# Performance work log

Measured on AMD Instinct MI355X. Metric: run time of the kernel, lower is better.

Reference implementation:

```python
import jax, jax.numpy as jnp
import numpy as np

D_MODEL = 2048
H = 8
DK = D_MODEL // H          # 256
EXPAND = 2
D_INNER = EXPAND * D_MODEL  # 4096
D_STATE = 16
D_CONV = 4
DT_RANK = D_MODEL // 16     # 128
B_SZ = 8
L = 1024


def setup_inputs() -> dict:
    key = jax.random.key(0)
    ks = jax.random.split(key, 20)
    s = 0.02
    inp = {
        "imageFeature": jax.random.normal(ks[0], (B_SZ, L, D_MODEL), jnp.float32),
        "kf": jax.random.normal(ks[1], (B_SZ, L, D_MODEL), jnp.float32),
        # MHA params (4 linears with bias)
        "Wq": jax.random.normal(ks[2], (D_MODEL, D_MODEL), jnp.float32) * s,
        "bq": jnp.zeros((D_MODEL,), jnp.float32),
        "Wk": jax.random.normal(ks[3], (D_MODEL, D_MODEL), jnp.float32) * s,
        "bk": jnp.zeros((D_MODEL,), jnp.float32),
        "Wv": jax.random.normal(ks[4], (D_MODEL, D_MODEL), jnp.float32) * s,
        "bv": jnp.zeros((D_MODEL,), jnp.float32),
        "Wo": jax.random.normal(ks[5], (D_MODEL, D_MODEL), jnp.float32) * s,
        "bo": jnp.zeros((D_MODEL,), jnp.float32),
        # Mamba params
        "W_in": jax.random.normal(ks[6], (D_MODEL, 2 * D_INNER), jnp.float32) * s,
        "conv_w": jax.random.normal(ks[7], (D_INNER, D_CONV), jnp.float32) * s,
        "conv_b": jnp.zeros((D_INNER,), jnp.float32),
        "W_extra": jax.random.normal(ks[8], (D_MODEL, D_INNER), jnp.float32) * s,
        "W_xproj": jax.random.normal(ks[9], (D_INNER, DT_RANK + 2 * D_STATE), jnp.float32) * s,
        "W_dt": jax.random.normal(ks[10], (DT_RANK, D_INNER), jnp.float32) * s,
        "b_dt": jnp.full((D_INNER,), -4.6, jnp.float32),  # softplus(-4.6) ~ 0.01 init dt
        "A_log": jnp.log(jnp.broadcast_to(jnp.arange(1, D_STATE + 1, dtype=jnp.float32), (D_INNER, D_STATE))),
        "D_skip": jnp.ones((D_INNER,), jnp.float32),
        "W_out": jax.random.normal(ks[11], (D_INNER, D_MODEL), jnp.float32) * s,
    }
    return inp


def _mha(x, Wq, bq, Wk, bk, Wv, bv, Wo, bo):
    B, T, _ = x.shape
    q = (x @ Wq + bq).reshape(B, T, H, DK)
    k = (x @ Wk + bk).reshape(B, T, H, DK)
    v = (x @ Wv + bv).reshape(B, T, H, DK)
    scores = jnp.einsum("bqhd,bkhd->bhqk", q, k) / jnp.sqrt(jnp.float32(DK))
    attn = jax.nn.softmax(scores, axis=-1)
    out = jnp.einsum("bhqk,bkhd->bqhd", attn, v).reshape(B, T, D_MODEL)
    return out @ Wo + bo


def _mamba_cross(x_in, kf, W_in, conv_w, conv_b, W_extra, W_xproj, W_dt, b_dt, A_log, D_skip, W_out):
    B, T, _ = x_in.shape
    xz = x_in @ W_in                       # (B,T,2*D_INNER)
    x, z = jnp.split(xz, 2, axis=-1)
    # causal depthwise conv1d (kernel D_CONV)
    x_pad = jnp.pad(x, ((0, 0), (D_CONV - 1, 0), (0, 0)))
    x_conv = sum(conv_w[:, k] * x_pad[:, k:k + T, :] for k in range(D_CONV)) + conv_b
    x = jax.nn.silu(x_conv)               # (B,T,D_INNER)
    # dt/B/C conditioned on extra_emb (cross path)
    e = kf @ W_extra                       # (B,T,D_INNER)
    dbc = e @ W_xproj                      # (B,T,DT_RANK+2*D_STATE)
    dt = jax.nn.softplus(dbc[..., :DT_RANK] @ W_dt + b_dt)        # (B,T,D_INNER)
    Bt = dbc[..., DT_RANK:DT_RANK + D_STATE]                      # (B,T,N)
    Ct = dbc[..., DT_RANK + D_STATE:]                             # (B,T,N)
    A = -jnp.exp(A_log)                    # (D_INNER, D_STATE)

    def step(h, inputs):
        x_t, dt_t, B_t, C_t = inputs       # (B,D),(B,D),(B,N),(B,N)
        dA = jnp.exp(dt_t[..., None] * A)              # (B,D,N)
        h = dA * h + dt_t[..., None] * B_t[:, None, :] * x_t[..., None]
        y_t = jnp.einsum("bdn,bn->bd", h, C_t)
        return h, y_t

    h0 = jnp.zeros((B, D_INNER, D_STATE), x.dtype)
    xs = (x.transpose(1, 0, 2), dt.transpose(1, 0, 2),
          Bt.transpose(1, 0, 2), Ct.transpose(1, 0, 2))
    _, ys = jax.lax.scan(step, h0, xs)     # ys: (T,B,D_INNER)
    y = ys.transpose(1, 0, 2) + D_skip * x
    y = y * jax.nn.silu(z)
    return y @ W_out


def reference(imageFeature, kf, Wq, bq, Wk, bk, Wv, bv, Wo, bo,
              W_in, conv_w, conv_b, W_extra, W_xproj, W_dt, b_dt,
              A_log, D_skip, W_out):
    att_feats = _mha(imageFeature, Wq, bq, Wk, bk, Wv, bv, Wo, bo)
    src = _mamba_cross(imageFeature, kf, W_in, conv_w, conv_b, W_extra,
                       W_xproj, W_dt, b_dt, A_log, D_skip, W_out)
    return jnp.stack([att_feats, src])     # (2,B,T,D_MODEL)
```

## Files before the change

kernel.cpp:

```cpp
#include <hip/hip_runtime.h>
#include <math.h>

#define NH 8
#define DKH 256
#define SEQ 1024
#define BSZ 8
#define DMODEL 2048
#define DINNER 4096
#define DSTATE 16
#define DTRANK 128

#define MiB 1048576ULL

#define O_XZ    (0*MiB)
#define O_IMGH  (256*MiB)
#define O_IMGL  (288*MiB)
#define O_WINTH (320*MiB)
#define O_WINTL (352*MiB)
#define O_WCOMB (384*MiB)
#define O_DBC   (384*MiB + 1310720ULL)
#define O_DT    (256*MiB)
#define O_YH    (256*MiB)
#define O_YL    (320*MiB)
#define O_WOUTH (0*MiB)
#define O_WOUTL (16*MiB)
#define A_IMGH  (0*MiB)
#define A_IMGL  (32*MiB)
#define A_WQH   (64*MiB)
#define A_WQL   (72*MiB)
#define A_WKH   (80*MiB)
#define A_WKL   (88*MiB)
#define A_WVH   (96*MiB)
#define A_WVL   (104*MiB)
#define A_WOH   (112*MiB)
#define A_WOL   (120*MiB)
#define A_QH    (128*MiB)
#define A_QL    (160*MiB)
#define A_KH    (192*MiB)
#define A_KL    (224*MiB)
#define A_VTH   (256*MiB)
#define A_VTL   (288*MiB)
#define A_S     (320*MiB)
#define A_ATTH  (0*MiB)
#define A_ATTL  (32*MiB)

#define FLAG_BIAS 1
#define FLAG_SOFTPLUS 2
#define FLAG_KT 4
#define FLAG_BF16 8

typedef __attribute__((ext_vector_type(8))) short bf16x8;
typedef __attribute__((ext_vector_type(4))) float f32x4;
typedef const void __attribute__((address_space(1))) gv_t;
typedef void __attribute__((address_space(3))) lv_t;

__device__ __forceinline__ unsigned short f2bf(float x) {
    unsigned u = __float_as_uint(x);
    unsigned r = u + 0x7FFFu + ((u >> 16) & 1u);
    return (unsigned short)(r >> 16);
}
__device__ __forceinline__ float bf2f(unsigned short h) {
    return __uint_as_float((unsigned)h << 16);
}

__global__ __launch_bounds__(256) void cvt_hilo(
    const float* __restrict__ in, unsigned short* __restrict__ hi,
    unsigned short* __restrict__ lo, int n4)
{
    int i = blockIdx.x * 256 + threadIdx.x;
    if (i >= n4) return;
    float4 x = ((const float4*)in)[i];
    ushort4 h, l;
    h.x = f2bf(x.x); l.x = f2bf(x.x - bf2f(h.x));
    h.y = f2bf(x.y); l.y = f2bf(x.y - bf2f(h.y));
    h.z = f2bf(x.z); l.z = f2bf(x.z - bf2f(h.z));
    h.w = f2bf(x.w); l.w = f2bf(x.w - bf2f(h.w));
    ((ushort4*)hi)[i] = h;
    ((ushort4*)lo)[i] = l;
}

__global__ __launch_bounds__(256) void tcvt(
    const float* __restrict__ W, unsigned short* __restrict__ Thi,
    unsigned short* __restrict__ Tlo, int K, int N)
{
    __shared__ float t[32][33];
    int tx = threadIdx.x & 31, ty = threadIdx.x >> 5;
    int k0 = blockIdx.y * 32, n0 = blockIdx.x * 32;
    #pragma unroll
    for (int i = 0; i < 32; i += 8)
        t[ty + i][tx] = W[(size_t)(k0 + ty + i) * N + n0 + tx];
    __syncthreads();
    #pragma unroll
    for (int i = 0; i < 32; i += 8) {
        float v = t[tx][ty + i];
        size_t o = (size_t)(n0 + ty + i) * K + k0 + tx;
        unsigned short h = f2bf(v);
        Thi[o] = h;
        Tlo[o] = f2bf(v - bf2f(h));
    }
}

__global__ __launch_bounds__(256) void ycvt(
    const float* __restrict__ xz, unsigned short* __restrict__ hi,
    unsigned short* __restrict__ lo)
{
    int i = blockIdx.x * 256 + threadIdx.x;
    int r = i >> 10, c4 = (i & 1023) << 2;
    float4 x = *(const float4*)&xz[(size_t)r * 8192 + c4];
    ushort4 h, l;
    h.x = f2bf(x.x); l.x = f2bf(x.x - bf2f(h.x));
    h.y = f2bf(x.y); l.y = f2bf(x.y - bf2f(h.y));
    h.z = f2bf(x.z); l.z = f2bf(x.z - bf2f(h.z));
    h.w = f2bf(x.w); l.w = f2bf(x.w - bf2f(h.w));
    size_t o = ((size_t)r * 4096 + c4) >> 2;
    ((ushort4*)hi)[o] = h;
    ((ushort4*)lo)[o] = l;
}

__device__ __forceinline__ void gload16(const unsigned short* g, unsigned short* l) {
    __builtin_amdgcn_global_load_lds((gv_t*)g, (lv_t*)l, 16, 0, 0);
}

__global__ __launch_bounds__(256) void gemm_mfma3(
    const unsigned short* __restrict__ Ahi, const unsigned short* __restrict__ Alo,
    const unsigned short* __restrict__ Bhi, const unsigned short* __restrict__ Blo,
    const float* __restrict__ bias, float* __restrict__ C,
    unsigned short* __restrict__ Chi, unsigned short* __restrict__ Clo,
    int M, int N, int K, int flags)
{
    __shared__ unsigned short sAh[128*32], sAl[128*32], sBh[128*32], sBl[128*32];
    int tid = threadIdx.x;
    int lane = tid & 63, wv = tid >> 6;
    int wm = wv >> 1, wn = wv & 1;
    int bm = blockIdx.y * 128, bn = blockIdx.x * 128;

    int rbase = wv * 32;
    int srow = lane >> 2;
    int scol = (lane & 3) * 8;
    const size_t aoff0 = (size_t)(bm + rbase + srow) * K + scol;
    const size_t aoff1 = aoff0 + (size_t)16 * K;
    const size_t boff0 = (size_t)(bn + rbase + srow) * K + scol;
    const size_t boff1 = boff0 + (size_t)16 * K;
    unsigned short* lA0 = &sAh[rbase * 32];
    unsigned short* lA1 = &sAh[(rbase + 16) * 32];
    unsigned short* lAl0 = &sAl[rbase * 32];
    unsigned short* lAl1 = &sAl[(rbase + 16) * 32];
    unsigned short* lB0 = &sBh[rbase * 32];
    unsigned short* lB1 = &sBh[(rbase + 16) * 32];
    unsigned short* lBl0 = &sBl[rbase * 32];
    unsigned short* lBl1 = &sBl[(rbase + 16) * 32];

    f32x4 acc[4][4];
    #pragma unroll
    for (int i = 0; i < 4; i++)
        #pragma unroll
        for (int j = 0; j < 4; j++)
            acc[i][j] = (f32x4){0.f, 0.f, 0.f, 0.f};

    int fr = lane & 15, q8 = (lane >> 4) * 8;

    for (int k0 = 0; k0 < K; k0 += 32) {
        gload16(Ahi + aoff0 + k0, lA0);
        gload16(Ahi + aoff1 + k0, lA1);
        gload16(Alo + aoff0 + k0, lAl0);
        gload16(Alo + aoff1 + k0, lAl1);
        gload16(Bhi + boff0 + k0, lB0);
        gload16(Bhi + boff1 + k0, lB1);
        gload16(Blo + boff0 + k0, lBl0);
        gload16(Blo + boff1 + k0, lBl1);
        __syncthreads();

        bf16x8 ah[4], al[4], bh[4], bl[4];
        #pragma unroll
        for (int t = 0; t < 4; t++) {
            ah[t] = *(const bf16x8*)&sAh[(wm * 64 + t * 16 + fr) * 32 + q8];
            al[t] = *(const bf16x8*)&sAl[(wm * 64 + t * 16 + fr) * 32 + q8];
            bh[t] = *(const bf16x8*)&sBh[(wn * 64 + t * 16 + fr) * 32 + q8];
            bl[t] = *(const bf16x8*)&sBl[(wn * 64 + t * 16 + fr) * 32 + q8];
        }
        #pragma unroll
        for (int i = 0; i < 4; i++)
            #pragma unroll
            for (int j = 0; j < 4; j++) {
                acc[i][j] = __builtin_amdgcn_mfma_f32_16x16x32_bf16(ah[i], bh[j], acc[i][j], 0, 0, 0);
                acc[i][j] = __builtin_amdgcn_mfma_f32_16x16x32_bf16(al[i], bh[j], acc[i][j], 0, 0, 0);
                acc[i][j] = __builtin_amdgcn_mfma_f32_16x16x32_bf16(ah[i], bl[j], acc[i][j], 0, 0, 0);
            }
        __syncthreads();
    }

    int q4 = (lane >> 4) * 4, c16 = lane & 15;
    #pragma unroll
    for (int i = 0; i < 4; i++)
        #pragma unroll
        for (int j = 0; j < 4; j++) {
            f32x4 v = acc[i][j];
            int col = bn + wn * 64 + j * 16 + c16;
            float bv = (flags & FLAG_BIAS) ? bias[col] : 0.f;
            #pragma unroll
            for (int r = 0; r < 4; r++) {
                int row = bm + wm * 64 + i * 16 + q4 + r;
                float val = v[r] + bv;
                if (flags & FLAG_BF16) {
                    size_t o;
                    if (flags & FLAG_KT) {
                        int bi = row >> 10, jj = row & 1023;
                        int hd = col >> 8, dk2 = col & 255;
                        o = ((size_t)((bi * NH + hd) * DKH + dk2)) * SEQ + jj;
                    } else {
                        o = (size_t)row * N + col;
                    }
                    unsigned short hv = f2bf(val);
                    Chi[o] = hv;
                    Clo[o] = f2bf(val - bf2f(hv));
                } else if (flags & FLAG_KT) {
                    int bi = row >> 10, jj = row & 1023;
                    int hd = col >> 8, dk2 = col & 255;
                    C[((size_t)((bi * NH + hd) * DKH + dk2)) * SEQ + jj] = val;
                } else {
                    C[(size_t)row * N + col] = val;
                }
            }
        }
}

__global__ __launch_bounds__(256) void gemm_att3(
    const unsigned short* __restrict__ Ahi, const unsigned short* __restrict__ Alo,
    const unsigned short* __restrict__ Bhi, const unsigned short* __restrict__ Blo,
    float* __restrict__ Cf, unsigned short* __restrict__ Ohi, unsigned short* __restrict__ Olo,
    int K, int lda, int ldb, int chunk_base, int mode)
{
    __shared__ unsigned short sAh[128*32], sAl[128*32], sBh[128*32], sBl[128*32];
    int tid = threadIdx.x;
    int lane = tid & 63, wv = tid >> 6;
    int wm = wv >> 1, wn = wv & 1;
    int bm = blockIdx.y * 128, bn = blockIdx.x * 128;
    int z = blockIdx.z;
    int g = chunk_base + z;

    size_t abase, bbase;
    if (mode == 0) {
        abase = (size_t)(g >> 3) * (1024 * 2048) + (size_t)(g & 7) * 256;
        bbase = abase;
    } else {
        abase = (size_t)z * (1024 * 2048);
        bbase = (size_t)g * (256 * 1024);
    }

    int rbase = wv * 32;
    int srow = lane >> 2;
    int scol = (lane & 3) * 8;
    const size_t aoff0 = abase + (size_t)(bm + rbase + srow) * lda + scol;
    const size_t aoff1 = aoff0 + (size_t)16 * lda;
    const size_t boff0 = bbase + (size_t)(bn + rbase + srow) * ldb + scol;
    const size_t boff1 = boff0 + (size_t)16 * ldb;
    unsigned short* lA0 = &sAh[rbase * 32];
    unsigned short* lA1 = &sAh[(rbase + 16) * 32];
    unsigned short* lAl0 = &sAl[rbase * 32];
    unsigned short* lAl1 = &sAl[(rbase + 16) * 32];
    unsigned short* lB0 = &sBh[rbase * 32];
    unsigned short* lB1 = &sBh[(rbase + 16) * 32];
    unsigned short* lBl0 = &sBl[rbase * 32];
    unsigned short* lBl1 = &sBl[(rbase + 16) * 32];

    f32x4 acc[4][4];
    #pragma unroll
    for (int i = 0; i < 4; i++)
        #pragma unroll
        for (int j = 0; j < 4; j++)
            acc[i][j] = (f32x4){0.f, 0.f, 0.f, 0.f};

    int fr = lane & 15, q8 = (lane >> 4) * 8;

    for (int k0 = 0; k0 < K; k0 += 32) {
        gload16(Ahi + aoff0 + k0, lA0);
        gload16(Ahi + aoff1 + k0, lA1);
        gload16(Alo + aoff0 + k0, lAl0);
        gload16(Alo + aoff1 + k0, lAl1);
        gload16(Bhi + boff0 + k0, lB0);
        gload16(Bhi + boff1 + k0, lB1);
        gload16(Blo + boff0 + k0, lBl0);
        gload16(Blo + boff1 + k0, lBl1);
        __syncthreads();

        bf16x8 ah[4], al[4], bh[4], bl[4];
        #pragma unroll
        for (int t = 0; t < 4; t++) {
            ah[t] = *(const bf16x8*)&sAh[(wm * 64 + t * 16 + fr) * 32 + q8];
            al[t] = *(const bf16x8*)&sAl[(wm * 64 + t * 16 + fr) * 32 + q8];
            bh[t] = *(const bf16x8*)&sBh[(wn * 64 + t * 16 + fr) * 32 + q8];
            bl[t] = *(const bf16x8*)&sBl[(wn * 64 + t * 16 + fr) * 32 + q8];
        }
        #pragma unroll
        for (int i = 0; i < 4; i++)
            #pragma unroll
            for (int j = 0; j < 4; j++) {
                acc[i][j] = __builtin_amdgcn_mfma_f32_16x16x32_bf16(ah[i], bh[j], acc[i][j], 0, 0, 0);
                acc[i][j] = __builtin_amdgcn_mfma_f32_16x16x32_bf16(al[i], bh[j], acc[i][j], 0, 0, 0);
                acc[i][j] = __builtin_amdgcn_mfma_f32_16x16x32_bf16(ah[i], bl[j], acc[i][j], 0, 0, 0);
            }
        __syncthreads();
    }

    int q4 = (lane >> 4) * 4, c16 = lane & 15;
    #pragma unroll
    for (int i = 0; i < 4; i++)
        #pragma unroll
        for (int j = 0; j < 4; j++) {
            f32x4 v = acc[i][j];
            int col = bn + wn * 64 + j * 16 + c16;
            #pragma unroll
            for (int r = 0; r < 4; r++) {
                int row = bm + wm * 64 + i * 16 + q4 + r;
                float val = v[r];
                if (mode == 0) {
                    Cf[(size_t)z * (1024 * 1024) + (size_t)row * 1024 + col] = val * 0.0625f;
                } else {
                    size_t o = ((size_t)((g >> 3) * 1024 + row)) * 2048 + (size_t)(g & 7) * 256 + col;
                    unsigned short hv = f2bf(val);
                    Ohi[o] = hv;
                    Olo[o] = f2bf(val - bf2f(hv));
                }
            }
        }
}

__global__ __launch_bounds__(256) void softmax_rows(float* __restrict__ S)
{
    int lane = threadIdx.x & 63, wid = threadIdx.x >> 6;
    size_t row = (size_t)blockIdx.x * 4 + wid;
    float* rp = S + row * 1024;

    float4 x[4];
    float m = -1e30f;
    #pragma unroll
    for (int w = 0; w < 4; w++) {
        x[w] = *(const float4*)&rp[w * 256 + lane * 4];
        m = fmaxf(m, fmaxf(fmaxf(x[w].x, x[w].y), fmaxf(x[w].z, x[w].w)));
    }
    #pragma unroll
    for (int off = 1; off < 64; off <<= 1) m = fmaxf(m, __shfl_xor(m, off));

    float s = 0.f;
    #pragma unroll
    for (int w = 0; w < 4; w++) {
        x[w].x = __expf(x[w].x - m);
        x[w].y = __expf(x[w].y - m);
        x[w].z = __expf(x[w].z - m);
        x[w].w = __expf(x[w].w - m);
        s += x[w].x + x[w].y + x[w].z + x[w].w;
    }
    #pragma unroll
    for (int off = 1; off < 64; off <<= 1) s += __shfl_xor(s, off);
    float inv = 1.f / s;

    unsigned short* hp = (unsigned short*)rp;
    unsigned short* lp = hp + 1024;
    #pragma unroll
    for (int w = 0; w < 4; w++) {
        float a0 = x[w].x * inv, a1 = x[w].y * inv;
        float a2 = x[w].z * inv, a3 = x[w].w * inv;
        ushort4 h, l;
        h.x = f2bf(a0); l.x = f2bf(a0 - bf2f(h.x));
        h.y = f2bf(a1); l.y = f2bf(a1 - bf2f(h.y));
        h.z = f2bf(a2); l.z = f2bf(a2 - bf2f(h.z));
        h.w = f2bf(a3); l.w = f2bf(a3 - bf2f(h.w));
        int c = w * 256 + lane * 4;
        *(ushort4*)&hp[c] = h;
        *(ushort4*)&lp[c] = l;
    }
}

#define BM 64
#define BN 64
#define BK 16
__global__ __launch_bounds__(256) void gemm_f32(
    const float* __restrict__ A, const float* __restrict__ B,
    const float* __restrict__ bias, float* __restrict__ C,
    int M, int N, int K, int lda, int ldb, int ldc, int flags)
{
    __shared__ float As[BK][BM + 4];
    __shared__ float Bs[BK][BN + 4];
    int tid = threadIdx.x;
    int tm = tid >> 4, tn = tid & 15;
    int bm = blockIdx.y * BM, bn = blockIdx.x * BN;
    float acc[4][4] = {};

    for (int k0 = 0; k0 < K; k0 += BK) {
        #pragma unroll
        for (int i = 0; i < 4; i++) {
            int idx = tid + i * 256;
            int r = idx >> 4, c = idx & 15;
            int gr = bm + r, gc = k0 + c;
            float v = 0.f;
            if (gr < M && gc < K) v = A[(size_t)gr * lda + gc];
            As[c][r] = v;
        }
        #pragma unroll
        for (int i = 0; i < 4; i++) {
            int idx = tid + i * 256;
            int r = idx >> 6, c = idx & 63;
            int gr = k0 + r, gc = bn + c;
            float v = 0.f;
            if (gr < K && gc < N) v = B[(size_t)gr * ldb + gc];
            Bs[r][c] = v;
        }
        __syncthreads();
        #pragma unroll
        for (int kk = 0; kk < BK; kk++) {
            float4 a4 = *(const float4*)&As[kk][tm * 4];
            float4 b4 = *(const float4*)&Bs[kk][tn * 4];
            float av[4] = {a4.x, a4.y, a4.z, a4.w};
            float bv[4] = {b4.x, b4.y, b4.z, b4.w};
            #pragma unroll
            for (int i = 0; i < 4; i++)
                #pragma unroll
                for (int j = 0; j < 4; j++)
                    acc[i][j] += av[i] * bv[j];
        }
        __syncthreads();
    }

    #pragma unroll
    for (int i = 0; i < 4; i++) {
        int row = bm + tm * 4 + i;
        if (row >= M) continue;
        #pragma unroll
        for (int j = 0; j < 4; j++) {
            int col = bn + tn * 4 + j;
            if (col >= N) continue;
            float val = acc[i][j];
            if (flags & FLAG_BIAS) val += bias[col];
            if (flags & FLAG_SOFTPLUS) val = (val > 20.f) ? val : log1pf(__expf(val));
            C[(size_t)row * ldc + col] = val;
        }
    }
}

__global__ __launch_bounds__(256) void mamba_scan(
    float* __restrict__ xz, const float* __restrict__ dt,
    const float* __restrict__ dbc, const float* __restrict__ A_log,
    const float* __restrict__ conv_w, const float* __restrict__ conv_b,
    const float* __restrict__ D_skip)
{
    int tid = threadIdx.x;
    int n = tid & 15;
    int dd = tid >> 4;
    int gb = blockIdx.x;
    int b = gb >> 8;
    int d = ((gb & 255) << 4) + dd;

    float A_n = -__expf(A_log[d * DSTATE + n]);
    float cw0 = conv_w[d * 4 + 0], cw1 = conv_w[d * 4 + 1];
    float cw2 = conv_w[d * 4 + 2], cw3 = conv_w[d * 4 + 3];
    float cb = conv_b[d];
    float dsk = D_skip[d];

    float h = 0.f;
    float w0 = 0.f, w1 = 0.f, w2 = 0.f;
    size_t rowx = (size_t)b * SEQ * 8192 + d;
    size_t rowdt = (size_t)b * SEQ * DINNER + d;
    size_t rowbc = (size_t)b * SEQ * 160;

    for (int t = 0; t < SEQ; t++) {
        float xr = xz[rowx + (size_t)t * 8192];
        float dtv = dt[rowdt + (size_t)t * DINNER];
        float Bv = dbc[rowbc + t * 160 + DTRANK + n];
        float Cv = dbc[rowbc + t * 160 + DTRANK + DSTATE + n];

        float xc = cw0 * w0 + cw1 * w1 + cw2 * w2 + cw3 * xr + cb;
        w0 = w1; w1 = w2; w2 = xr;
        float xs = xc / (1.f + __expf(-xc));

        float dA = __expf(dtv * A_n);
        h = dA * h + dtv * Bv * xs;
        float p = h * Cv;
        p += __shfl_xor(p, 1, 16);
        p += __shfl_xor(p, 2, 16);
        p += __shfl_xor(p, 4, 16);
        p += __shfl_xor(p, 8, 16);

        float y = p + dsk * xs;
        float zv = xz[rowx + (size_t)t * 8192 + DINNER];
        y = y * (zv / (1.f + __expf(-zv)));
        if (n == 0) xz[rowx + (size_t)t * 8192] = y;
    }
}

extern "C" void kernel_launch(void* const* d_in, const int* in_sizes, int n_in,
                              void* d_out, int out_size, void* d_ws, size_t ws_size,
                              hipStream_t stream) {
    const float* imgF   = (const float*)d_in[0];
    const float* kf     = (const float*)d_in[1];
    const float* Wq     = (const float*)d_in[2];
    const float* bq     = (const float*)d_in[3];
    const float* Wk     = (const float*)d_in[4];
    const float* bk     = (const float*)d_in[5];
    const float* Wv     = (const float*)d_in[6];
    const float* bv     = (const float*)d_in[7];
    const float* Wo     = (const float*)d_in[8];
    const float* bo     = (const float*)d_in[9];
    const float* W_in   = (const float*)d_in[10];
    const float* conv_w = (const float*)d_in[11];
    const float* conv_b = (const float*)d_in[12];
    const float* W_extra= (const float*)d_in[13];
    const float* W_xproj= (const float*)d_in[14];
    const float* W_dt   = (const float*)d_in[15];
    const float* b_dt   = (const float*)d_in[16];
    const float* A_log  = (const float*)d_in[17];
    const float* D_skip = (const float*)d_in[18];
    const float* W_out  = (const float*)d_in[19];
    float* out = (float*)d_out;
    char* W = (char*)d_ws;

    #define WS_F(off) ((float*)(W + (off)))
    #define WS_U(off) ((unsigned short*)(W + (off)))

    dim3 blk(256);
    auto gg = [](int M, int N) { return dim3((N + BN - 1) / BN, (M + BM - 1) / BM); };

    cvt_hilo<<<dim3(16384), blk, 0, stream>>>(imgF, WS_U(O_IMGH), WS_U(O_IMGL), 4194304);
    tcvt<<<dim3(8192/32, 2048/32), blk, 0, stream>>>(W_in, WS_U(O_WINTH), WS_U(O_WINTL), 2048, 8192);
    gemm_mfma3<<<dim3(64, 64), blk, 0, stream>>>(WS_U(O_IMGH), WS_U(O_IMGL),
        WS_U(O_WINTH), WS_U(O_WINTL), nullptr, WS_F(O_XZ), nullptr, nullptr,
        8192, 8192, 2048, 0);
    gemm_f32<<<gg(2048, 160), blk, 0, stream>>>(W_extra, W_xproj, nullptr, WS_F(O_WCOMB),
        2048, 160, 4096, 4096, 160, 160, 0);
    gemm_f32<<<gg(8192, 160), blk, 0, stream>>>(kf, WS_F(O_WCOMB), nullptr, WS_F(O_DBC),
        8192, 160, 2048, 2048, 160, 160, 0);
    gemm_f32<<<gg(8192, 4096), blk, 0, stream>>>(WS_F(O_DBC), W_dt, b_dt, WS_F(O_DT),
        8192, 4096, 128, 160, 4096, 4096, FLAG_BIAS | FLAG_SOFTPLUS);
    mamba_scan<<<dim3(2048), blk, 0, stream>>>(WS_F(O_XZ), WS_F(O_DT), WS_F(O_DBC),
        A_log, conv_w, conv_b, D_skip);
    ycvt<<<dim3(32768), blk, 0, stream>>>(WS_F(O_XZ), WS_U(O_YH), WS_U(O_YL));
    tcvt<<<dim3(2048/32, 4096/32), blk, 0, stream>>>(W_out, WS_U(O_WOUTH), WS_U(O_WOUTL), 4096, 2048);
    gemm_mfma3<<<dim3(16, 64), blk, 0, stream>>>(WS_U(O_YH), WS_U(O_YL),
        WS_U(O_WOUTH), WS_U(O_WOUTL), nullptr, out + 16777216, nullptr, nullptr,
        8192, 2048, 4096, 0);

    cvt_hilo<<<dim3(16384), blk, 0, stream>>>(imgF, WS_U(A_IMGH), WS_U(A_IMGL), 4194304);
    tcvt<<<dim3(64, 64), blk, 0, stream>>>(Wq, WS_U(A_WQH), WS_U(A_WQL), 2048, 2048);
    tcvt<<<dim3(64, 64), blk, 0, stream>>>(Wk, WS_U(A_WKH), WS_U(A_WKL), 2048, 2048);
    tcvt<<<dim3(64, 64), blk, 0, stream>>>(Wv, WS_U(A_WVH), WS_U(A_WVL), 2048, 2048);
    tcvt<<<dim3(64, 64), blk, 0, stream>>>(Wo, WS_U(A_WOH), WS_U(A_WOL), 2048, 2048);
    gemm_mfma3<<<dim3(16, 64), blk, 0, stream>>>(WS_U(A_IMGH), WS_U(A_IMGL),
        WS_U(A_WQH), WS_U(A_WQL), bq, nullptr, WS_U(A_QH), WS_U(A_QL),
        8192, 2048, 2048, FLAG_BIAS | FLAG_BF16);
    gemm_mfma3<<<dim3(16, 64), blk, 0, stream>>>(WS_U(A_IMGH), WS_U(A_IMGL),
        WS_U(A_WKH), WS_U(A_WKL), bk, nullptr, WS_U(A_KH), WS_U(A_KL),
        8192, 2048, 2048, FLAG_BIAS | FLAG_BF16);
    gemm_mfma3<<<dim3(16, 64), blk, 0, stream>>>(WS_U(A_IMGH), WS_U(A_IMGL),
        WS_U(A_WVH), WS_U(A_WVL), bv, nullptr, WS_U(A_VTH), WS_U(A_VTL),
        8192, 2048, 2048, FLAG_BIAS | FLAG_BF16 | FLAG_KT);
    for (int c = 0; c < 4; c++) {
        gemm_att3<<<dim3(8, 8, 16), blk, 0, stream>>>(WS_U(A_QH), WS_U(A_QL),
            WS_U(A_KH), WS_U(A_KL), WS_F(A_S), nullptr, nullptr,
            256, 2048, 2048, c * 16, 0);
        softmax_rows<<<dim3(4096), blk, 0, stream>>>(WS_F(A_S));
        gemm_att3<<<dim3(2, 8, 16), blk, 0, stream>>>(
            (unsigned short*)WS_F(A_S), (unsigned short*)WS_F(A_S) + 1024,
            WS_U(A_VTH), WS_U(A_VTL), nullptr, WS_U(A_ATTH), WS_U(A_ATTL),
            1024, 2048, 1024, c * 16, 1);
    }
    gemm_mfma3<<<dim3(16, 64), blk, 0, stream>>>(WS_U(A_ATTH), WS_U(A_ATTL),
        WS_U(A_WOH), WS_U(A_WOL), bo, out, nullptr, nullptr,
        8192, 2048, 2048, FLAG_BIAS);
}
```

Before: 5.500 ms.

## Hoist conv and SiLU out of Mamba scan into parallel prep kernel

A new scan_prep kernel computes the causal depthwise conv plus SiLU and the gate SiLU in parallel over time chunks. It writes xs into the not-yet-used output buffer and the gated z back in place. B and C are repacked interleaved so the scan loads them with one float2. The serial scan then does only the recurrence, using DPP row reductions instead of shuffles, and is unrolled by two. This shortens the latency-bound serial loop, at the cost of an extra pass over memory and of using the output region as scratch.

```diff
diff --git a/kernel.cpp b/kernel.cpp
--- a/kernel.cpp
+++ b/kernel.cpp
@@ -63,6 +63,16 @@
     return __uint_as_float((unsigned)h << 16);
 }
 
+__device__ __forceinline__ float fsilu(float x) {
+    return x * __builtin_amdgcn_rcpf(1.f + __expf(-x));
+}
+
+template<int CTRL>
+__device__ __forceinline__ float dppadd(float x) {
+    return x + __int_as_float(__builtin_amdgcn_mov_dpp(
+        __float_as_int(x), CTRL, 0xf, 0xf, true));
+}
+
 __global__ __launch_bounds__(256) void cvt_hilo(
     const float* __restrict__ in, unsigned short* __restrict__ hi,
     unsigned short* __restrict__ lo, int n4)
@@ -437,11 +447,50 @@
     }
 }
 
+__global__ __launch_bounds__(256) void repack_bc(float* __restrict__ dbc)
+{
+    int i = blockIdx.x * 256 + threadIdx.x;
+    int n = i & 15;
+    int row = i >> 4;
+    float B = dbc[(size_t)row * 160 + DTRANK + n];
+    float C = dbc[(size_t)row * 160 + DTRANK + DSTATE + n];
+    float2 p; p.x = B; p.y = C;
+    ((float2*)&dbc[(size_t)row * 160])[n] = p;
+}
+
+__global__ __launch_bounds__(256) void scan_prep(
+    const float* __restrict__ xz_r, float* __restrict__ xz_w,
+    const float* __restrict__ conv_w, const float* __restrict__ conv_b,
+    float* __restrict__ xs_out)
+{
+    int d = blockIdx.x * 256 + threadIdx.x;
+    int t0 = blockIdx.y * 128;
+    int b = blockIdx.z;
+    float cw0 = conv_w[d * 4 + 0], cw1 = conv_w[d * 4 + 1];
+    float cw2 = conv_w[d * 4 + 2], cw3 = conv_w[d * 4 + 3];
+    float cb = conv_b[d];
+    size_t base = (size_t)b * SEQ * 8192 + d;
+
+    float w0 = 0.f, w1 = 0.f, w2 = 0.f;
+    if (t0 > 0) {
+        w0 = xz_r[base + (size_t)(t0 - 3) * 8192];
+        w1 = xz_r[base + (size_t)(t0 - 2) * 8192];
+        w2 = xz_r[base + (size_t)(t0 - 1) * 8192];
+    }
+    for (int t = t0; t < t0 + 128; t++) {
+        float xr = xz_r[base + (size_t)t * 8192];
+        float xc = cw0 * w0 + cw1 * w1 + cw2 * w2 + cw3 * xr + cb;
+        w0 = w1; w1 = w2; w2 = xr;
+        xs_out[((size_t)b * SEQ + t) * 4096 + d] = fsilu(xc);
+        float zv = xz_r[base + (size_t)t * 8192 + DINNER];
+        xz_w[base + (size_t)t * 8192 + DINNER] = fsilu(zv);
+    }
+}
+
 __global__ __launch_bounds__(256) void mamba_scan(
     float* __restrict__ xz, const float* __restrict__ dt,
-    const float* __restrict__ dbc, const float* __restrict__ A_log,
-    const float* __restrict__ conv_w, const float* __restrict__ conv_b,
-    const float* __restrict__ D_skip)
+    const float* __restrict__ bc, const float* __restrict__ A_log,
+    const float* __restrict__ D_skip, const float* __restrict__ xs)
 {
     int tid = threadIdx.x;
     int n = tid & 15;
@@ -451,39 +500,31 @@
     int d = ((gb & 255) << 4) + dd;
 
     float A_n = -__expf(A_log[d * DSTATE + n]);
-    float cw0 = conv_w[d * 4 + 0], cw1 = conv_w[d * 4 + 1];
-    float cw2 = conv_w[d * 4 + 2], cw3 = conv_w[d * 4 + 3];
-    float cb = conv_b[d];
     float dsk = D_skip[d];
 
     float h = 0.f;
-    float w0 = 0.f, w1 = 0.f, w2 = 0.f;
     size_t rowx = (size_t)b * SEQ * 8192 + d;
-    size_t rowdt = (size_t)b * SEQ * DINNER + d;
+    size_t rowd = (size_t)b * SEQ * 4096 + d;
     size_t rowbc = (size_t)b * SEQ * 160;
 
+    #pragma unroll 2
     for (int t = 0; t < SEQ; t++) {
-        float xr = xz[rowx + (size_t)t * 8192];
-        float dtv = dt[rowdt + (size_t)t * DINNER];
-        float Bv = dbc[rowbc + t * 160 + DTRANK + n];
-        float Cv = dbc[rowbc + t * 160 + DTRANK + DSTATE + n];
-
-        float xc = cw0 * w0 + cw1 * w1 + cw2 * w2 + cw3 * xr + cb;
-        w0 = w1; w1 = w2; w2 = xr;
-        float xs = xc / (1.f + __expf(-xc));
+        float xv  = xs[rowd + (size_t)t * 4096];
+        float dtv = dt[rowd + (size_t)t * 4096];
+        float2 bcv = *(const float2*)&bc[rowbc + (size_t)t * 160 + 2 * n];
+        float g   = xz[rowx + (size_t)t * 8192 + DINNER];
 
         float dA = __expf(dtv * A_n);
-        h = dA * h + dtv * Bv * xs;
-        float p = h * Cv;
-        p += __shfl_xor(p, 1, 16);
-        p += __shfl_xor(p, 2, 16);
-        p += __shfl_xor(p, 4, 16);
-        p += __shfl_xor(p, 8, 16);
-
-        float y = p + dsk * xs;
-        float zv = xz[rowx + (size_t)t * 8192 + DINNER];
-        y = y * (zv / (1.f + __expf(-zv)));
-        if (n == 0) xz[rowx + (size_t)t * 8192] = y;
+        h = dA * h + (dtv * xv) * bcv.x;
+        float p = h * bcv.y;
+        p = dppadd<0xB1>(p);
+        p = dppadd<0x4E>(p);
+        p = dppadd<0x141>(p);
+        p = dppadd<0x140>(p);
+        if (n == 0) {
+            float y = (p + dsk * xv) * g;
+            xz[rowx + (size_t)t * 8192] = y;
+        }
     }
 }
 
@@ -530,8 +571,11 @@
         8192, 160, 2048, 2048, 160, 160, 0);
     gemm_f32<<<gg(8192, 4096), blk, 0, stream>>>(WS_F(O_DBC), W_dt, b_dt, WS_F(O_DT),
         8192, 4096, 128, 160, 4096, 4096, FLAG_BIAS | FLAG_SOFTPLUS);
+    repack_bc<<<dim3(512), blk, 0, stream>>>(WS_F(O_DBC));
+    scan_prep<<<dim3(16, 8, 8), blk, 0, stream>>>(WS_F(O_XZ), WS_F(O_XZ),
+        conv_w, conv_b, out);
     mamba_scan<<<dim3(2048), blk, 0, stream>>>(WS_F(O_XZ), WS_F(O_DT), WS_F(O_DBC),
-        A_log, conv_w, conv_b, D_skip);
+        A_log, D_skip, out);
     ycvt<<<dim3(32768), blk, 0, stream>>>(WS_F(O_XZ), WS_U(O_YH), WS_U(O_YL));
     tcvt<<<dim3(2048/32, 4096/32), blk, 0, stream>>>(W_out, WS_U(O_WOUTH), WS_U(O_WOUTL), 4096, 2048);
     gemm_mfma3<<<dim3(16, 64), blk, 0, stream>>>(WS_U(O_YH), WS_U(O_YL),
```

After: 5.367 ms. 1.02x faster.
